# Kernel tuning notes

Hardware: AMD Instinct MI355X
Metric: run time of the kernel (lower is better)

The kernel has to match this reference:

```python
import jax, jax.numpy as jnp
import numpy as np

ALPHA = 1.0
BETA = 1.0


def setup_inputs() -> dict:
    key = jax.random.key(0)
    k1, k2, k3, k4 = jax.random.split(key, 4)
    B_, S, D_in, D_out, R = 4, 64, 8192, 8192, 16
    x = jax.random.normal(k1, (B_, S, D_in), dtype=jnp.float32)
    original_weight = jax.random.normal(k2, (D_out, D_in), dtype=jnp.float32) * 0.02
    A = jax.random.normal(k3, (D_out, R), dtype=jnp.float32) * 0.02
    Bm = jax.random.normal(k4, (R, D_in), dtype=jnp.float32) * 0.02
    return {"x": x, "original_weight": original_weight, "A": A, "B": Bm}


def reference(x, original_weight, A, B):
    # delta_weight = alpha * (A @ B)  -> [D_out, D_in]
    delta_weight = ALPHA * jnp.matmul(A, B)
    # F.linear(x, W + beta*delta) = x @ (W + beta*delta)^T
    W = original_weight + BETA * delta_weight
    return jnp.einsum("bsd,od->bso", x, W)
```

## Files before the change

kernel.cpp:

```cpp
#include <hip/hip_runtime.h>
#include <stdint.h>


#define DM 256
#define DK 8192
#define DN 8192
#define RLORA 16

#define TN 64
#define BK 64
#define KSPLIT 4
#define KCHUNK (DK / KSPLIT)
#define NITER (KCHUNK / BK)

typedef short bf16x8 __attribute__((ext_vector_type(8)));
typedef float f32x4v __attribute__((ext_vector_type(4)));

typedef __attribute__((address_space(1))) const unsigned char glbc_u8;
typedef __attribute__((address_space(3))) unsigned char lds_u8;

__device__ __forceinline__ unsigned short f2bf(float f) {
  unsigned u = __builtin_bit_cast(unsigned, f);
  u += 0x7FFFu + ((u >> 16) & 1u);
  return (unsigned short)(u >> 16);
}

__global__ __launch_bounds__(256) void prep_x_y(
    const float* __restrict__ x, const float* __restrict__ Bm,
    unsigned short* __restrict__ xb, unsigned short* __restrict__ yb) {
  const int m = blockIdx.x;
  const int tid = threadIdx.x;
  const float4* xrow = (const float4*)(x + (size_t)m * DK);
  unsigned short* xbrow = xb + (size_t)m * DK;
  float acc[RLORA];
#pragma unroll
  for (int r = 0; r < RLORA; ++r) acc[r] = 0.f;
  for (int j = tid; j < DK / 4; j += 256) {
    float4 v = xrow[j];
    ushort4 h;
    h.x = f2bf(v.x); h.y = f2bf(v.y); h.z = f2bf(v.z); h.w = f2bf(v.w);
    *(ushort4*)(xbrow + j * 4) = h;
#pragma unroll
    for (int r = 0; r < RLORA; ++r) {
      float4 b = ((const float4*)(Bm + (size_t)r * DK))[j];
      acc[r] += v.x * b.x + v.y * b.y + v.z * b.z + v.w * b.w;
    }
  }
  __shared__ float red[256 * RLORA];
#pragma unroll
  for (int r = 0; r < RLORA; ++r) red[tid * RLORA + r] = acc[r];
  __syncthreads();
  for (int off = 128; off >= 1; off >>= 1) {
    if (tid < off) {
#pragma unroll
      for (int r = 0; r < RLORA; ++r)
        red[tid * RLORA + r] += red[(tid + off) * RLORA + r];
    }
    __syncthreads();
  }
  if (tid < 64)
    yb[m * 64 + tid] = (tid < RLORA) ? f2bf(red[tid]) : (unsigned short)0;
}

__global__ __launch_bounds__(256) void prep_A(
    const float* __restrict__ A, unsigned short* __restrict__ Ab) {
  const int base = blockIdx.x * 1024 + threadIdx.x;
#pragma unroll
  for (int i = 0; i < 4; ++i) {
    int e = base + i * 256;
    int n = e >> 6, c = e & 63;
    Ab[e] = (c < RLORA) ? f2bf(A[n * RLORA + c]) : (unsigned short)0;
  }
}

__global__ __launch_bounds__(256, 2) void lora_gemm(
    const unsigned short* __restrict__ xb,
    const float* __restrict__ W,
    const unsigned short* __restrict__ yb,
    const unsigned short* __restrict__ Ab,
    float* __restrict__ out) {
  __shared__ unsigned short xs[DM * BK];
  __shared__ unsigned short wt[TN * BK];

  const int tid = threadIdx.x;
  const int lane = tid & 63;
  const int wave = tid >> 6;
  const int n_base = blockIdx.x * TN;
  const int kz = blockIdx.y;
  const int k_base = kz * KCHUNK;

  f32x4v acc[4][4];
#pragma unroll
  for (int mi = 0; mi < 4; ++mi)
#pragma unroll
    for (int ni = 0; ni < 4; ++ni) acc[mi][ni] = {0.f, 0.f, 0.f, 0.f};

  const unsigned short* xgp[8];
#pragma unroll
  for (int j = 0; j < 8; ++j) {
    int idx = wave * 512 + j * 64 + lane;
    int r = idx & 15, c = (idx >> 4) & 3, s = (idx >> 6) & 1, g = idx >> 7;
    xgp[j] = xb + (size_t)(g * 16 + r) * DK + k_base + s * 32 + c * 8;
  }
  const float4* wgp[2];
  unsigned wlds[2];
#pragma unroll
  for (int j = 0; j < 2; ++j) {
    int idx = j * 256 + tid;
    int r = idx & 15, c = (idx >> 4) & 3, s = (idx >> 6) & 1, g = idx >> 7;
    wgp[j] = (const float4*)(W + (size_t)(n_base + g * 16 + r) * DK +
                             k_base + s * 32 + c * 8);
    wlds[j] = idx * 16;
  }

  const int niter = (kz == 0) ? NITER + 1 : NITER;

  for (int it = 0; it < niter; ++it) {
    const bool lora = (it == NITER);
    if (!lora) {
      float4 wv0[2], wv1[2];
#pragma unroll
      for (int j = 0; j < 2; ++j) { wv0[j] = wgp[j][0]; wv1[j] = wgp[j][1]; wgp[j] += BK / 4; }
#pragma unroll
      for (int j = 0; j < 8; ++j) {
        __builtin_amdgcn_global_load_lds(
            (glbc_u8*)xgp[j],
            (lds_u8*)((char*)xs + (wave * 512 + j * 64) * 16), 16, 0, 0);
        xgp[j] += BK;
      }
#pragma unroll
      for (int j = 0; j < 2; ++j) {
        uint4 p;
        p.x = (unsigned)f2bf(wv0[j].x) | ((unsigned)f2bf(wv0[j].y) << 16);
        p.y = (unsigned)f2bf(wv0[j].z) | ((unsigned)f2bf(wv0[j].w) << 16);
        p.z = (unsigned)f2bf(wv1[j].x) | ((unsigned)f2bf(wv1[j].y) << 16);
        p.w = (unsigned)f2bf(wv1[j].z) | ((unsigned)f2bf(wv1[j].w) << 16);
        *(uint4*)((char*)wt + wlds[j]) = p;
      }
    } else {
#pragma unroll
      for (int j = 0; j < 8; ++j) {
        int idx = wave * 512 + j * 64 + lane;
        int r = idx & 15, c = (idx >> 4) & 3, s = (idx >> 6) & 1, g = idx >> 7;
        const unsigned short* gp = yb + (g * 16 + r) * 64 + s * 32 + c * 8;
        __builtin_amdgcn_global_load_lds(
            (glbc_u8*)gp, (lds_u8*)((char*)xs + (wave * 512 + j * 64) * 16), 16, 0, 0);
      }
#pragma unroll
      for (int j = 0; j < 2; ++j) {
        int idx = wave * 128 + j * 64 + lane;
        int r = idx & 15, c = (idx >> 4) & 3, s = (idx >> 6) & 1, g = idx >> 7;
        const unsigned short* gp = Ab + (size_t)(n_base + g * 16 + r) * 64 + s * 32 + c * 8;
        __builtin_amdgcn_global_load_lds(
            (glbc_u8*)gp, (lds_u8*)((char*)wt + (wave * 128 + j * 64) * 16), 16, 0, 0);
      }
    }
    __syncthreads();

#pragma unroll
    for (int s = 0; s < 2; ++s) {
      bf16x8 a[4], b[4];
#pragma unroll
      for (int mi = 0; mi < 4; ++mi) {
        int g = wave * 4 + mi;
        a[mi] = *(const bf16x8*)((const char*)xs + ((g * 2 + s) * 64 + lane) * 16);
      }
#pragma unroll
      for (int ni = 0; ni < 4; ++ni)
        b[ni] = *(const bf16x8*)((const char*)wt + ((ni * 2 + s) * 64 + lane) * 16);
#pragma unroll
      for (int mi = 0; mi < 4; ++mi)
#pragma unroll
        for (int ni = 0; ni < 4; ++ni)
          acc[mi][ni] = __builtin_amdgcn_mfma_f32_16x16x32_bf16(
              a[mi], b[ni], acc[mi][ni], 0, 0, 0);
    }
    __syncthreads();
  }

  const int row0 = (lane >> 4) * 4;
  const int col = lane & 15;
#pragma unroll
  for (int mi = 0; mi < 4; ++mi)
#pragma unroll
    for (int ni = 0; ni < 4; ++ni)
#pragma unroll
      for (int rg = 0; rg < 4; ++rg) {
        int m = wave * 64 + mi * 16 + row0 + rg;
        int n = n_base + ni * 16 + col;
        atomicAdd(out + (size_t)m * DN + n, acc[mi][ni][rg]);
      }
}

extern "C" void kernel_launch(void* const* d_in, const int* in_sizes, int n_in,
                              void* d_out, int out_size, void* d_ws, size_t ws_size,
                              hipStream_t stream) {
  const float* x  = (const float*)d_in[0];
  const float* W  = (const float*)d_in[1];
  const float* A  = (const float*)d_in[2];
  const float* Bm = (const float*)d_in[3];
  float* out = (float*)d_out;

  unsigned short* xb = (unsigned short*)d_ws;
  unsigned short* yb = xb + (size_t)DM * DK;
  unsigned short* Ab = yb + (size_t)DM * 64;

  hipMemsetAsync(d_out, 0, (size_t)out_size * sizeof(float), stream);
  prep_x_y<<<DM, 256, 0, stream>>>(x, Bm, xb, yb);
  prep_A<<<512, 256, 0, stream>>>(A, Ab);
  lora_gemm<<<dim3(DN / TN, KSPLIT), 256, 0, stream>>>(xb, W, yb, Ab, out);
}
```

Measured before the change: 457.8 us.

## Restructure LoRA GEMM: register-fed W fragments, double-buffered x, split-K partial buffers

The GEMM now uses 8 waves with 128-column tiles and split-K of 8. Each wave converts its own W slice straight from registers into MFMA B operands, with the next slice prefetched, so W no longer goes through LDS. The x tile is double-buffered in LDS through async global-to-LDS loads, and the LoRA A operand is read directly from fp32 A. Partial sums go to a workspace buffer that a separate pass reduces, falling back to atomics when the workspace is too small. The x/B prep is parallelised over K with wave shuffles and atomics. The cost is more launches and a large partial buffer whose read and write traffic competes with the main kernel.

```diff
diff --git a/kernel.cpp b/kernel.cpp
--- a/kernel.cpp
+++ b/kernel.cpp
@@ -7,9 +7,9 @@
 #define DN 8192
 #define RLORA 16
 
-#define TN 64
+#define TN 128
 #define BK 64
-#define KSPLIT 4
+#define KSPLIT 8
 #define KCHUNK (DK / KSPLIT)
 #define NITER (KCHUNK / BK)
 
@@ -25,171 +25,195 @@
   return (unsigned short)(u >> 16);
 }
 
-__global__ __launch_bounds__(256) void prep_x_y(
+__device__ __forceinline__ bf16x8 pack8(float4 a, float4 b) {
+  bf16x8 r;
+  r[0] = (short)f2bf(a.x); r[1] = (short)f2bf(a.y);
+  r[2] = (short)f2bf(a.z); r[3] = (short)f2bf(a.w);
+  r[4] = (short)f2bf(b.x); r[5] = (short)f2bf(b.y);
+  r[6] = (short)f2bf(b.z); r[7] = (short)f2bf(b.w);
+  return r;
+}
+
+__global__ __launch_bounds__(256) void prep_x(
     const float* __restrict__ x, const float* __restrict__ Bm,
-    unsigned short* __restrict__ xb, unsigned short* __restrict__ yb) {
-  const int m = blockIdx.x;
-  const int tid = threadIdx.x;
-  const float4* xrow = (const float4*)(x + (size_t)m * DK);
-  unsigned short* xbrow = xb + (size_t)m * DK;
-  float acc[RLORA];
-#pragma unroll
-  for (int r = 0; r < RLORA; ++r) acc[r] = 0.f;
-  for (int j = tid; j < DK / 4; j += 256) {
-    float4 v = xrow[j];
+    unsigned short* __restrict__ xb, float* __restrict__ y32) {
+  const int ks = blockIdx.x;
+  const int m0 = blockIdx.y * 4;
+  const int t = threadIdx.x;
+  const int k0 = ks * 1024 + t * 4;
+  float4 xv[4];
+#pragma unroll
+  for (int i = 0; i < 4; ++i) {
+    xv[i] = *(const float4*)(x + (size_t)(m0 + i) * DK + k0);
     ushort4 h;
-    h.x = f2bf(v.x); h.y = f2bf(v.y); h.z = f2bf(v.z); h.w = f2bf(v.w);
-    *(ushort4*)(xbrow + j * 4) = h;
-#pragma unroll
-    for (int r = 0; r < RLORA; ++r) {
-      float4 b = ((const float4*)(Bm + (size_t)r * DK))[j];
-      acc[r] += v.x * b.x + v.y * b.y + v.z * b.z + v.w * b.w;
-    }
-  }
-  __shared__ float red[256 * RLORA];
-#pragma unroll
-  for (int r = 0; r < RLORA; ++r) red[tid * RLORA + r] = acc[r];
+    h.x = f2bf(xv[i].x); h.y = f2bf(xv[i].y);
+    h.z = f2bf(xv[i].z); h.w = f2bf(xv[i].w);
+    *(ushort4*)(xb + (size_t)(m0 + i) * DK + k0) = h;
+  }
+  float acc[4][RLORA];
+#pragma unroll
+  for (int r = 0; r < RLORA; ++r) {
+    float4 b = *(const float4*)(Bm + (size_t)r * DK + k0);
+#pragma unroll
+    for (int i = 0; i < 4; ++i)
+      acc[i][r] = xv[i].x * b.x + xv[i].y * b.y + xv[i].z * b.z + xv[i].w * b.w;
+  }
+#pragma unroll
+  for (int off = 32; off >= 1; off >>= 1)
+#pragma unroll
+    for (int i = 0; i < 4; ++i)
+#pragma unroll
+      for (int r = 0; r < RLORA; ++r)
+        acc[i][r] += __shfl_xor(acc[i][r], off, 64);
+  __shared__ float red[4][4][RLORA];
+  const int lane = t & 63, wv = t >> 6;
+  if (lane == 0) {
+#pragma unroll
+    for (int i = 0; i < 4; ++i)
+#pragma unroll
+      for (int r = 0; r < RLORA; ++r) red[wv][i][r] = acc[i][r];
+  }
   __syncthreads();
-  for (int off = 128; off >= 1; off >>= 1) {
-    if (tid < off) {
-#pragma unroll
-      for (int r = 0; r < RLORA; ++r)
-        red[tid * RLORA + r] += red[(tid + off) * RLORA + r];
-    }
-    __syncthreads();
-  }
-  if (tid < 64)
-    yb[m * 64 + tid] = (tid < RLORA) ? f2bf(red[tid]) : (unsigned short)0;
-}
-
-__global__ __launch_bounds__(256) void prep_A(
-    const float* __restrict__ A, unsigned short* __restrict__ Ab) {
-  const int base = blockIdx.x * 1024 + threadIdx.x;
-#pragma unroll
-  for (int i = 0; i < 4; ++i) {
-    int e = base + i * 256;
-    int n = e >> 6, c = e & 63;
-    Ab[e] = (c < RLORA) ? f2bf(A[n * RLORA + c]) : (unsigned short)0;
-  }
-}
-
-__global__ __launch_bounds__(256, 2) void lora_gemm(
+  if (t < 64) {
+    int i = t >> 4, r = t & 15;
+    float s = red[0][i][r] + red[1][i][r] + red[2][i][r] + red[3][i][r];
+    atomicAdd(y32 + (m0 + i) * RLORA + r, s);
+  }
+}
+
+__global__ __launch_bounds__(256) void pack_y(
+    const float* __restrict__ y32, unsigned short* __restrict__ yb) {
+  int e = blockIdx.x * 256 + threadIdx.x;
+  int m = e >> 6, c = e & 63;
+  yb[e] = (c < RLORA) ? f2bf(y32[m * RLORA + c]) : (unsigned short)0;
+}
+
+__global__ __launch_bounds__(512, 4) void lora_gemm(
     const unsigned short* __restrict__ xb,
     const float* __restrict__ W,
     const unsigned short* __restrict__ yb,
-    const unsigned short* __restrict__ Ab,
-    float* __restrict__ out) {
-  __shared__ unsigned short xs[DM * BK];
-  __shared__ unsigned short wt[TN * BK];
+    const float* __restrict__ A,
+    float* __restrict__ out,
+    float* __restrict__ part) {
+  __shared__ unsigned short xs[2][DM * BK];
 
   const int tid = threadIdx.x;
   const int lane = tid & 63;
   const int wave = tid >> 6;
-  const int n_base = blockIdx.x * TN;
+  const int nb = blockIdx.x * TN;
   const int kz = blockIdx.y;
-  const int k_base = kz * KCHUNK;
-
-  f32x4v acc[4][4];
-#pragma unroll
-  for (int mi = 0; mi < 4; ++mi)
-#pragma unroll
-    for (int ni = 0; ni < 4; ++ni) acc[mi][ni] = {0.f, 0.f, 0.f, 0.f};
-
-  const unsigned short* xgp[8];
-#pragma unroll
-  for (int j = 0; j < 8; ++j) {
-    int idx = wave * 512 + j * 64 + lane;
+  const int kb = kz * KCHUNK;
+  const int n0 = nb + wave * 16;
+  const int qr = lane & 15;
+  const int quad = lane >> 4;
+
+  const unsigned short* xgp[4];
+  unsigned xdst[4];
+#pragma unroll
+  for (int j = 0; j < 4; ++j) {
+    int idx = (wave * 4 + j) * 64 + lane;
     int r = idx & 15, c = (idx >> 4) & 3, s = (idx >> 6) & 1, g = idx >> 7;
-    xgp[j] = xb + (size_t)(g * 16 + r) * DK + k_base + s * 32 + c * 8;
-  }
-  const float4* wgp[2];
-  unsigned wlds[2];
-#pragma unroll
-  for (int j = 0; j < 2; ++j) {
-    int idx = j * 256 + tid;
-    int r = idx & 15, c = (idx >> 4) & 3, s = (idx >> 6) & 1, g = idx >> 7;
-    wgp[j] = (const float4*)(W + (size_t)(n_base + g * 16 + r) * DK +
-                             k_base + s * 32 + c * 8);
-    wlds[j] = idx * 16;
-  }
-
-  const int niter = (kz == 0) ? NITER + 1 : NITER;
+    xgp[j] = xb + (size_t)(g * 16 + r) * DK + kb + s * 32 + c * 8;
+    xdst[j] = (unsigned)((wave * 4 + j) * 1024);
+  }
+  const float* wp = W + (size_t)(n0 + qr) * DK + kb + quad * 8;
+
+  f32x4v acc[16];
+#pragma unroll
+  for (int g = 0; g < 16; ++g) acc[g] = (f32x4v){0.f, 0.f, 0.f, 0.f};
+
+  const bool isLora = (kz == 0);
+  const int niter = isLora ? NITER + 1 : NITER;
+
+  float4 f0 = *(const float4*)(wp);
+  float4 f1 = *(const float4*)(wp + 4);
+  float4 f2 = *(const float4*)(wp + 32);
+  float4 f3 = *(const float4*)(wp + 36);
+  wp += BK;
+#pragma unroll
+  for (int j = 0; j < 4; ++j) {
+    __builtin_amdgcn_global_load_lds((glbc_u8*)xgp[j],
+        (lds_u8*)((char*)&xs[0][0] + xdst[j]), 16, 0, 0);
+    xgp[j] += BK;
+  }
+  __syncthreads();
 
   for (int it = 0; it < niter; ++it) {
-    const bool lora = (it == NITER);
-    if (!lora) {
-      float4 wv0[2], wv1[2];
-#pragma unroll
-      for (int j = 0; j < 2; ++j) { wv0[j] = wgp[j][0]; wv1[j] = wgp[j][1]; wgp[j] += BK / 4; }
-#pragma unroll
-      for (int j = 0; j < 8; ++j) {
-        __builtin_amdgcn_global_load_lds(
-            (glbc_u8*)xgp[j],
-            (lds_u8*)((char*)xs + (wave * 512 + j * 64) * 16), 16, 0, 0);
+    const int cur = it & 1, nxt = (it + 1) & 1;
+    const int ni = it + 1;
+    if (ni < NITER) {
+#pragma unroll
+      for (int j = 0; j < 4; ++j) {
+        __builtin_amdgcn_global_load_lds((glbc_u8*)xgp[j],
+            (lds_u8*)((char*)&xs[nxt][0] + xdst[j]), 16, 0, 0);
         xgp[j] += BK;
       }
-#pragma unroll
-      for (int j = 0; j < 2; ++j) {
-        uint4 p;
-        p.x = (unsigned)f2bf(wv0[j].x) | ((unsigned)f2bf(wv0[j].y) << 16);
-        p.y = (unsigned)f2bf(wv0[j].z) | ((unsigned)f2bf(wv0[j].w) << 16);
-        p.z = (unsigned)f2bf(wv1[j].x) | ((unsigned)f2bf(wv1[j].y) << 16);
-        p.w = (unsigned)f2bf(wv1[j].z) | ((unsigned)f2bf(wv1[j].w) << 16);
-        *(uint4*)((char*)wt + wlds[j]) = p;
-      }
-    } else {
-#pragma unroll
-      for (int j = 0; j < 8; ++j) {
-        int idx = wave * 512 + j * 64 + lane;
+    } else if (ni == NITER && isLora) {
+#pragma unroll
+      for (int j = 0; j < 4; ++j) {
+        int idx = (wave * 4 + j) * 64 + lane;
         int r = idx & 15, c = (idx >> 4) & 3, s = (idx >> 6) & 1, g = idx >> 7;
         const unsigned short* gp = yb + (g * 16 + r) * 64 + s * 32 + c * 8;
-        __builtin_amdgcn_global_load_lds(
-            (glbc_u8*)gp, (lds_u8*)((char*)xs + (wave * 512 + j * 64) * 16), 16, 0, 0);
+        __builtin_amdgcn_global_load_lds((glbc_u8*)gp,
+            (lds_u8*)((char*)&xs[nxt][0] + xdst[j]), 16, 0, 0);
       }
-#pragma unroll
-      for (int j = 0; j < 2; ++j) {
-        int idx = wave * 128 + j * 64 + lane;
-        int r = idx & 15, c = (idx >> 4) & 3, s = (idx >> 6) & 1, g = idx >> 7;
-        const unsigned short* gp = Ab + (size_t)(n_base + g * 16 + r) * 64 + s * 32 + c * 8;
-        __builtin_amdgcn_global_load_lds(
-            (glbc_u8*)gp, (lds_u8*)((char*)wt + (wave * 128 + j * 64) * 16), 16, 0, 0);
-      }
+    }
+    bf16x8 b0 = pack8(f0, f1);
+    bf16x8 b1 = pack8(f2, f3);
+    if (ni < NITER) {
+      f0 = *(const float4*)(wp);
+      f1 = *(const float4*)(wp + 4);
+      f2 = *(const float4*)(wp + 32);
+      f3 = *(const float4*)(wp + 36);
+      wp += BK;
+    } else if (ni == NITER && isLora) {
+      const float* ap = A + (size_t)(n0 + qr) * RLORA + quad * 8;
+      float4 z = {0.f, 0.f, 0.f, 0.f};
+      f0 = (quad < 2) ? *(const float4*)(ap) : z;
+      f1 = (quad < 2) ? *(const float4*)(ap + 4) : z;
+      f2 = z; f3 = z;
+    }
+    const char* xbase = (const char*)&xs[cur][0];
+#pragma unroll
+    for (int g = 0; g < 16; ++g) {
+      bf16x8 a = *(const bf16x8*)(xbase + ((g * 2 + 0) * 64 + lane) * 16);
+      acc[g] = __builtin_amdgcn_mfma_f32_16x16x32_bf16(a, b0, acc[g], 0, 0, 0);
+    }
+#pragma unroll
+    for (int g = 0; g < 16; ++g) {
+      bf16x8 a = *(const bf16x8*)(xbase + ((g * 2 + 1) * 64 + lane) * 16);
+      acc[g] = __builtin_amdgcn_mfma_f32_16x16x32_bf16(a, b1, acc[g], 0, 0, 0);
     }
     __syncthreads();
-
-#pragma unroll
-    for (int s = 0; s < 2; ++s) {
-      bf16x8 a[4], b[4];
-#pragma unroll
-      for (int mi = 0; mi < 4; ++mi) {
-        int g = wave * 4 + mi;
-        a[mi] = *(const bf16x8*)((const char*)xs + ((g * 2 + s) * 64 + lane) * 16);
-      }
-#pragma unroll
-      for (int ni = 0; ni < 4; ++ni)
-        b[ni] = *(const bf16x8*)((const char*)wt + ((ni * 2 + s) * 64 + lane) * 16);
-#pragma unroll
-      for (int mi = 0; mi < 4; ++mi)
-#pragma unroll
-        for (int ni = 0; ni < 4; ++ni)
-          acc[mi][ni] = __builtin_amdgcn_mfma_f32_16x16x32_bf16(
-              a[mi], b[ni], acc[mi][ni], 0, 0, 0);
-    }
-    __syncthreads();
-  }
-
-  const int row0 = (lane >> 4) * 4;
-  const int col = lane & 15;
-#pragma unroll
-  for (int mi = 0; mi < 4; ++mi)
-#pragma unroll
-    for (int ni = 0; ni < 4; ++ni)
-#pragma unroll
-      for (int rg = 0; rg < 4; ++rg) {
-        int m = wave * 64 + mi * 16 + row0 + rg;
-        int n = n_base + ni * 16 + col;
-        atomicAdd(out + (size_t)m * DN + n, acc[mi][ni][rg]);
-      }
+  }
+
+  if (part) {
+    float* pb = part + (size_t)kz * DM * DN + n0 + (lane & 15);
+#pragma unroll
+    for (int g = 0; g < 16; ++g)
+#pragma unroll
+      for (int rg = 0; rg < 4; ++rg)
+        pb[(size_t)(g * 16 + quad * 4 + rg) * DN] = acc[g][rg];
+  } else {
+    float* ob = out + n0 + (lane & 15);
+#pragma unroll
+    for (int g = 0; g < 16; ++g)
+#pragma unroll
+      for (int rg = 0; rg < 4; ++rg)
+        atomicAdd(ob + (size_t)(g * 16 + quad * 4 + rg) * DN, acc[g][rg]);
+  }
+}
+
+__global__ __launch_bounds__(256) void reduce_k(
+    const float* __restrict__ part, float* __restrict__ out) {
+  size_t i = ((size_t)blockIdx.x * 256 + threadIdx.x) * 4;
+  float4 s = *(const float4*)(part + i);
+#pragma unroll
+  for (int kz = 1; kz < KSPLIT; ++kz) {
+    float4 v = *(const float4*)(part + (size_t)kz * DM * DN + i);
+    s.x += v.x; s.y += v.y; s.z += v.z; s.w += v.w;
+  }
+  *(float4*)(out + i) = s;
 }
 
 extern "C" void kernel_launch(void* const* d_in, const int* in_sizes, int n_in,
@@ -203,10 +227,17 @@
 
   unsigned short* xb = (unsigned short*)d_ws;
   unsigned short* yb = xb + (size_t)DM * DK;
-  unsigned short* Ab = yb + (size_t)DM * 64;
+  float* y32 = (float*)(yb + (size_t)DM * 64);
+  size_t base_bytes = (size_t)DM * DK * 2 + (size_t)DM * 64 * 2 +
+                      (size_t)DM * RLORA * 4;
+  size_t part_bytes = (size_t)KSPLIT * DM * DN * 4;
+  bool use_part = ws_size >= base_bytes + part_bytes;
+  float* part = use_part ? (float*)((char*)d_ws + base_bytes) : nullptr;
 
   hipMemsetAsync(d_out, 0, (size_t)out_size * sizeof(float), stream);
-  prep_x_y<<<DM, 256, 0, stream>>>(x, Bm, xb, yb);
-  prep_A<<<512, 256, 0, stream>>>(A, Ab);
-  lora_gemm<<<dim3(DN / TN, KSPLIT), 256, 0, stream>>>(xb, W, yb, Ab, out);
-}
+  hipMemsetAsync(y32, 0, (size_t)DM * RLORA * sizeof(float), stream);
+  prep_x<<<dim3(8, 64), 256, 0, stream>>>(x, Bm, xb, y32);
+  pack_y<<<64, 256, 0, stream>>>(y32, yb);
+  lora_gemm<<<dim3(DN / TN, KSPLIT), 512, 0, stream>>>(xb, W, yb, A, out, part);
+  if (use_part) reduce_k<<<2048, 256, 0, stream>>>(part, out);
+}
```

New measurement: 467.0 us. 1.02x slower.
